# Kernel optimization log

Measured on AMD Instinct MI355X. Metric: run time of the kernel, lower is better.

Reference implementation:

```python
import jax, jax.numpy as jnp
import numpy as np


def _resize_axis(x, axis, out_size):
    # PyTorch bilinear interpolate, align_corners=False, no antialias (half-pixel centers)
    in_size = x.shape[axis]
    src = (jnp.arange(out_size) + 0.5) * (in_size / out_size) - 0.5
    src = jnp.clip(src, 0.0, in_size - 1.0)
    lo = jnp.floor(src).astype(jnp.int32)
    hi = jnp.minimum(lo + 1, in_size - 1)
    w = (src - lo).astype(x.dtype)
    shp = [1] * x.ndim
    shp[axis] = out_size
    w = w.reshape(shp)
    return jnp.take(x, lo, axis=axis) * (1 - w) + jnp.take(x, hi, axis=axis) * w


def _bilinear(x, h, w):
    return _resize_axis(_resize_axis(x, 2, h), 3, w)


def _unfold3(x):
    # F.unfold(kernel_size=3, padding=1) -> [B, C, 9, H*W], kernel offsets row-major
    B, C, H, W = x.shape
    xp = jnp.pad(x, ((0, 0), (0, 0), (1, 1), (1, 1)))
    pats = jnp.stack([xp[:, :, dy:dy + H, dx:dx + W] for dy in range(3) for dx in range(3)], axis=2)
    return pats.reshape(B, C, 9, H * W)


def setup_inputs() -> dict:
    key = jax.random.key(0)
    ks = jax.random.split(key, 7)
    B, C, H, W = 4, 64, 192, 192
    return {
        "x": jax.random.normal(ks[0], (B, C, H, W), jnp.float32),
        "gn_weight": jnp.ones((C,), jnp.float32) + 0.1 * jax.random.normal(ks[1], (C,), jnp.float32),
        "gn_bias": 0.1 * jax.random.normal(ks[2], (C,), jnp.float32),
        "w1": jax.random.normal(ks[3], (2 * C, C), jnp.float32) / np.sqrt(C).astype(np.float32),
        "b1": 0.01 * jax.random.normal(ks[4], (2 * C,), jnp.float32),
        "w2": jax.random.normal(ks[5], (C, 2 * C), jnp.float32) / np.sqrt(2 * C).astype(np.float32),
        "b2": 0.01 * jax.random.normal(ks[6], (C,), jnp.float32),
    }


def reference(x, gn_weight, gn_bias, w1, b1, w2, b2):
    B, C, H, W = x.shape
    MIN_CONN, MAX_CONN, THRESHOLD, POWER = 1, 16, 0.3, 2
    KSQ = 9
    K_MAX = min(MAX_CONN, KSQ)
    EPS_NORM = 1e-12

    x_down = _bilinear(x, H // 2, W // 2)
    x_du = _bilinear(x_down, H, W)
    df = jnp.abs(x - x_du).sum(1, keepdims=True)            # [B,1,H,W]
    dmin = df.reshape(B, -1).min(1).reshape(B, 1, 1, 1)
    dmax = df.reshape(B, -1).max(1).reshape(B, 1, 1, 1)
    dfp = ((df - dmin) / (dmax - dmin + 1e-8)) ** POWER
    mask = (dfp > THRESHOLD).astype(x.dtype)
    conn = MIN_CONN + jnp.clip(jnp.round(dfp * (MAX_CONN - MIN_CONN)), 0) * mask
    counts = conn.reshape(B, H * W)                          # [B,HW]
    process = counts > 1

    # ---- per-pixel cosine similarity to 3x3 neighborhood ----
    patches = _unfold3(x)                                    # [B,C,9,HW]
    x_flat = x.reshape(B, C, H * W)
    xn = x_flat / jnp.maximum(jnp.linalg.norm(x_flat, axis=1, keepdims=True), EPS_NORM)
    pn = patches / jnp.maximum(jnp.linalg.norm(patches, axis=1, keepdims=True), EPS_NORM)
    sim = jnp.einsum('bcn,bckn->bkn', xn, pn)                # [B,9,HW]

    # ---- adaptive top-k (k = min(count, 9)) + exp-softmax weighted sum of raw patches ----
    order = jnp.argsort(-sim, axis=1)                        # descending over the 9 neighbors
    sim_s = jnp.take_along_axis(sim, order, axis=1)
    pat_s = jnp.take_along_axis(patches, jnp.broadcast_to(order[:, None], patches.shape), axis=2)
    k = jnp.minimum(counts, K_MAX)                           # [B,HW]
    keep = (jnp.arange(KSQ)[None, :, None] < k[:, None, :]).astype(x.dtype)
    wts = jnp.exp(sim_s) * keep
    wts = wts / jnp.maximum(wts.sum(1, keepdims=True), EPS_NORM)
    weighted = jnp.einsum('bckn,bkn->bcn', pat_s, wts)       # [B,C,HW]
    output = jnp.where(process[:, None, :], weighted, x_flat).reshape(B, C, H, W)

    # ---- GroupNorm(32, C) on identity ----
    G = 32
    xg = x.reshape(B, G, C // G, H, W)
    mu = xg.mean((2, 3, 4), keepdims=True)
    var = xg.var((2, 3, 4), keepdims=True)
    nx = ((xg - mu) / jnp.sqrt(var + 1e-5)).reshape(B, C, H, W)
    norm_x = nx * gn_weight[None, :, None, None] + gn_bias[None, :, None, None]

    enhanced = output + norm_x
    # ---- conv_ffn: 1x1 conv C->2C, ReLU, 1x1 conv 2C->C ----
    h1 = jax.nn.relu(jnp.einsum('oc,bchw->bohw', w1, enhanced) + b1[None, :, None, None])
    ffn = jnp.einsum('oc,bchw->bohw', w2, h1) + b2[None, :, None, None]
    return enhanced + ffn
```

## Files before the change

### kernel.cpp

```cpp
#include <hip/hip_runtime.h>
#include <hip/hip_bf16.h>

#define BB 4
#define CC 64
#define HH 192
#define WW 192
#define HWSZ (HH*WW)
#define HD 96
#define WD 96
#define GG 32
#define FTH 512
#define FPX 128
#define FBPB (HWSZ/FPX)
#define PBLK 128
#define BPB (HWSZ/PBLK)

typedef short short8 __attribute__((ext_vector_type(8)));
typedef float f32x4  __attribute__((ext_vector_type(4)));

__device__ __forceinline__ unsigned short f2bf(float f) {
    unsigned u = __float_as_uint(f);
    return (unsigned short)((u + 0x7FFFu + ((u >> 16) & 1u)) >> 16);
}
__device__ __forceinline__ float bf2f(unsigned short s) {
    return __uint_as_float(((unsigned)s) << 16);
}
__device__ __forceinline__ unsigned pk2(float a, float b) {
    return (unsigned)f2bf(a) | ((unsigned)f2bf(b) << 16);
}
__device__ __forceinline__ short8 u4s8(uint4 u) {
    union { uint4 a; short8 b; } cvt; cvt.a = u; return cvt.b;
}

__device__ __forceinline__ int swz1152(int bid) {
    return (bid & 7) * 144 + (bid >> 3);
}

__global__ __launch_bounds__(512) void k_init(const float* __restrict__ w1,
                                              const float* __restrict__ w2,
                                              unsigned* __restrict__ wf,
                                              float* __restrict__ gnacc,
                                              unsigned* __restrict__ mm) {
    int tid = threadIdx.x;
    if (blockIdx.x == 0) {
        if (tid < 256) gnacc[tid] = 0.f;
        if (tid < 2*BB) mm[tid] = (tid & 1) ? 0u : 0x7F800000u;
    }
    int i = blockIdx.x*512 + tid;
    if (i < 4096) {
        float2 v = ((const float2*)w1)[i];
        int j = i >> 5, cp = i & 31, c0 = cp << 1;
        int fi = ((j >> 4) << 1) + (c0 >> 5);
        int ln = (((c0 & 31) >> 3) << 4) + (j & 15);
        wf[fi*256 + ln*4 + (cp & 3)] = pk2(v.x, v.y);
    } else {
        int i2 = i - 4096;
        float2 v = ((const float2*)w2)[i2];
        int c = i2 >> 6, jp = i2 & 63, j0 = jp << 1;
        int fi = ((j0 >> 5) << 2) + (c >> 4);
        int ln = (((j0 & 31) >> 3) << 4) + (c & 15);
        wf[4096 + fi*256 + ln*4 + (jp & 3)] = pk2(v.x, v.y);
    }
}

__global__ __launch_bounds__(256) void k_pre(const float* __restrict__ x,
                                             float* __restrict__ df,
                                             float* __restrict__ nrm,
                                             float* __restrict__ gnacc,
                                             unsigned* __restrict__ mm) {
    __shared__ float sgn[64];
    __shared__ float wmn[4], wmx[4];
    int tid = threadIdx.x;
    if (tid < 64) sgn[tid] = 0.f;
    __syncthreads();

    int virt = swz1152(blockIdx.x);
    int b = virt / BPB;
    int pb = (virt % BPB) * PBLK;
    int wave = tid >> 6, lane = tid & 63;
    int oct = lane >> 3, grp = lane & 7;
    int p0 = pb + wave*32 + grp*4;
    int h = p0 / WW, w0 = p0 % WW;

    float hs = fminf(fmaxf(0.5f*(float)h - 0.25f, 0.f), 95.f);
    int hl = (int)hs; int hh2 = min(hl+1, 95); float fh = hs - (float)hl;
    int r0 = 2*hl, r1 = 2*hh2;

    int t0 = min(max(w0/2 - 1, 0), 92);
    float wc[4][4];
    #pragma unroll
    for (int i = 0; i < 4; ++i) {
        float wsr = fminf(fmaxf(0.5f*(float)(w0+i) - 0.25f, 0.f), 95.f);
        int wl = (int)wsr; int wh = min(wl+1, 95); float fw = wsr - (float)wl;
        int kl = wl - t0, kh = wh - t0;
        #pragma unroll
        for (int k = 0; k < 4; ++k)
            wc[i][k] = ((k==kl) ? (1.f-fw) : 0.f) + ((k==kh) ? fw : 0.f);
    }

    const float* xb = x + (size_t)b*CC*HWSZ;
    float d[4]  = {0.f,0.f,0.f,0.f};
    float qn[4] = {0.f,0.f,0.f,0.f};
    float gs[4] = {0.f,0.f,0.f,0.f};
    float gq[4] = {0.f,0.f,0.f,0.f};
    #pragma unroll
    for (int cc = 0; cc < 8; ++cc) {
        const float* pc = xb + (size_t)(oct*8 + cc)*HWSZ;
        float4 xc = *(const float4*)(pc + h*WW + w0);
        const float* pa = pc + r0*WW + 2*t0;
        const float* pq = pc + r1*WW + 2*t0;
        float T[4];
        #pragma unroll
        for (int k = 0; k < 4; ++k) {
            float2 a0 = *(const float2*)(pa + 2*k);
            float2 a1 = *(const float2*)(pa + WW + 2*k);
            float2 c0 = *(const float2*)(pq + 2*k);
            float2 c1 = *(const float2*)(pq + WW + 2*k);
            float xdA = 0.25f*((a0.x + a1.x) + (a0.y + a1.y));
            float xdB = 0.25f*((c0.x + c1.x) + (c0.y + c1.y));
            T[k] = (1.f-fh)*xdA + fh*xdB;
        }
        float xv[4] = {xc.x, xc.y, xc.z, xc.w};
        float sch = 0.f, qch = 0.f;
        #pragma unroll
        for (int i = 0; i < 4; ++i) {
            float du = (wc[i][0]*T[0] + wc[i][1]*T[1]) + (wc[i][2]*T[2] + wc[i][3]*T[3]);
            d[i] += fabsf(xv[i] - du);
            float x2 = xv[i]*xv[i];
            qn[i] += x2;
            sch += xv[i];
            qch += x2;
        }
        gs[cc>>1] += sch;
        gq[cc>>1] += qch;
    }
    #pragma unroll
    for (int o = 8; o <= 32; o <<= 1) {
        #pragma unroll
        for (int i = 0; i < 4; ++i) {
            d[i]  += __shfl_xor(d[i], o);
            qn[i] += __shfl_xor(qn[i], o);
        }
    }
    if (oct == 0) {
        *(float4*)(df  + (size_t)b*HWSZ + p0) = make_float4(d[0], d[1], d[2], d[3]);
        *(float4*)(nrm + (size_t)b*HWSZ + p0) =
            make_float4(sqrtf(qn[0]), sqrtf(qn[1]), sqrtf(qn[2]), sqrtf(qn[3]));
    }
    float mn = fminf(fminf(d[0], d[1]), fminf(d[2], d[3]));
    float mx = fmaxf(fmaxf(d[0], d[1]), fmaxf(d[2], d[3]));
    #pragma unroll
    for (int o = 1; o < 64; o <<= 1) {
        mn = fminf(mn, __shfl_xor(mn, o));
        mx = fmaxf(mx, __shfl_xor(mx, o));
    }
    if (lane == 0) { wmn[wave] = mn; wmx[wave] = mx; }
    #pragma unroll
    for (int o = 1; o <= 4; o <<= 1) {
        #pragma unroll
        for (int j = 0; j < 4; ++j) {
            gs[j] += __shfl_xor(gs[j], o);
            gq[j] += __shfl_xor(gq[j], o);
        }
    }
    if (grp == 0) {
        #pragma unroll
        for (int j = 0; j < 4; ++j) {
            atomicAdd(&sgn[2*(oct*4+j)],   gs[j]);
            atomicAdd(&sgn[2*(oct*4+j)+1], gq[j]);
        }
    }
    __syncthreads();
    if (tid < 64) atomicAdd(&gnacc[(size_t)b*64 + tid], sgn[tid]);
    if (tid == 0) {
        float bmn = fminf(fminf(wmn[0], wmn[1]), fminf(wmn[2], wmn[3]));
        float bmx = fmaxf(fmaxf(wmx[0], wmx[1]), fmaxf(wmx[2], wmx[3]));
        atomicMin(&mm[2*b],   __float_as_uint(bmn));
        atomicMax(&mm[2*b+1], __float_as_uint(bmx));
    }
}

__global__ __launch_bounds__(FTH, 4) void k_fused(const float* __restrict__ x,
                                                  const float* __restrict__ df,
                                                  const float* __restrict__ nrm,
                                                  const unsigned* __restrict__ mm,
                                                  const float* __restrict__ gnacc,
                                                  const float* __restrict__ gw,
                                                  const float* __restrict__ gb,
                                                  const unsigned* __restrict__ wf,
                                                  const float* __restrict__ b1,
                                                  const float* __restrict__ b2,
                                                  float* __restrict__ out) {
    __shared__ __align__(16) unsigned char lds[24576];
    unsigned* se = (unsigned*)lds;
    unsigned* sh = (unsigned*)(lds + 16384);
    float* gnv = (float*)(lds + 16384);

    int tid = threadIdx.x;
    int wv = tid >> 6, lane = tid & 63;
    int q = lane >> 4, m = lane & 15;

    int virt = swz1152(blockIdx.x);
    int b = virt / FBPB;
    int pb = (virt % FBPB) * FPX;
    int pxl = wv*16 + m;
    int p = pb + pxl;
    int h = p / WW, w = p % WW;
    int cbase = q*16;

    if (tid < 32) {
        float n = 2.f*HWSZ;
        float mu  = gnacc[(size_t)b*64 + 2*tid] / n;
        float var = gnacc[(size_t)b*64 + 2*tid + 1] / n - mu*mu;
        gnv[2*tid]   = mu;
        gnv[2*tid+1] = rsqrtf(var + 1e-5f);
    }
    __syncthreads();

    float dmin = __uint_as_float(mm[2*b]);
    float dmax = __uint_as_float(mm[2*b+1]);
    float dfp = (df[b*HWSZ+p] - dmin) / (dmax - dmin + 1e-8f);
    dfp = dfp * dfp;
    bool maskv = dfp > 0.3f;
    float conn = 1.f + (maskv ? fmaxf(rintf(dfp * 15.f), 0.f) : 0.f);
    bool process = conn > 1.f;
    int kk = (int)fminf(conn, 9.f);

    const float* xb = x + (size_t)b*CC*HWSZ + p;
    const int dhv[9] = {-1,-1,-1, 0,0,0, 1,1,1};
    const int dwv[9] = {-1, 0, 1,-1,0,1,-1,0,1};
    bool valid[9]; int offc[9];
    #pragma unroll
    for (int j = 0; j < 9; ++j) {
        int hn = h + dhv[j], wn = w + dwv[j];
        valid[j] = (hn >= 0) && (hn < HH) && (wn >= 0) && (wn < WW);
        offc[j] = valid[j] ? (dhv[j]*WW + dwv[j]) : 0;
    }
    float wtc[9];
    #pragma unroll
    for (int j = 0; j < 9; ++j) wtc[j] = 0.f;

    if (process) {
        float dot[9];
        #pragma unroll
        for (int j = 0; j < 9; ++j) dot[j] = 0.f;
        #pragma unroll 2
        for (int cc = 0; cc < 16; ++cc) {
            const float* pc = xb + (size_t)(cbase + cc)*HWSZ;
            float xc = pc[0];
            #pragma unroll
            for (int j = 0; j < 9; ++j)
                dot[j] += xc * pc[offc[j]];
        }
        #pragma unroll
        for (int j = 0; j < 9; ++j) {
            dot[j] += __shfl_xor(dot[j], 16);
            dot[j] += __shfl_xor(dot[j], 32);
        }
        float nc = fmaxf(nrm[b*HWSZ+p], 1e-12f);
        float sim[9];
        #pragma unroll
        for (int j = 0; j < 9; ++j) {
            float nj = fmaxf(nrm[b*HWSZ+p+offc[j]], 1e-12f);
            sim[j] = valid[j] ? dot[j] / (nc * nj) : 0.f;
        }
        float S = 0.f;
        float wt[9];
        #pragma unroll
        for (int j = 0; j < 9; ++j) {
            int rank = 0;
            #pragma unroll
            for (int l = 0; l < 9; ++l)
                rank += (sim[l] > sim[j]) || (sim[l] == sim[j] && l < j);
            float ex = (rank < kk) ? expf(sim[j]) : 0.f;
            wt[j] = ex; S += ex;
        }
        float inv = 1.f / fmaxf(S, 1e-12f);
        #pragma unroll
        for (int j = 0; j < 9; ++j)
            wtc[j] = valid[j] ? wt[j] * inv : 0.f;
    }

    float e[16];
    for (int cc = 0; cc < 16; ++cc) {
        int c = cbase + cc;
        const float* pc = xb + (size_t)c*HWSZ;
        float xc = pc[0];
        float oc;
        if (process) {
            float a = 0.f;
            #pragma unroll
            for (int j = 0; j < 9; ++j)
                a += wtc[j] * pc[offc[j]];
            oc = a;
        } else oc = xc;
        int g = c >> 1;
        float mu = gnv[2*g], is = gnv[2*g+1];
        e[cc] = oc + (xc - mu) * is * gw[c] + gb[c];
    }

    {
        int kc = q >> 1, qo = q & 1;
        unsigned* dst = se + (wv*2 + kc)*256;
        int la = 32*qo + m;
        uint4 ua, ub;
        ua.x = pk2(e[0],e[1]);  ua.y = pk2(e[2],e[3]);
        ua.z = pk2(e[4],e[5]);  ua.w = pk2(e[6],e[7]);
        ub.x = pk2(e[8],e[9]);  ub.y = pk2(e[10],e[11]);
        ub.z = pk2(e[12],e[13]); ub.w = pk2(e[14],e[15]);
        *(uint4*)(dst + la*4)      = ua;
        *(uint4*)(dst + (la+16)*4) = ub;
    }
    __syncthreads();

    const unsigned* wf1g = wf;
    const unsigned* wf2g = wf + 4096;
    int n16 = m;
    float b1v[8], b2v[4];
    #pragma unroll
    for (int nt = 0; nt < 8; ++nt) b1v[nt] = b1[nt*16 + n16];
    #pragma unroll
    for (int n2 = 0; n2 < 4; ++n2) b2v[n2] = b2[n2*16 + n16];

    uint4 a0 = *(uint4*)(se + (wv*2+0)*256 + lane*4);
    uint4 a1 = *(uint4*)(se + (wv*2+1)*256 + lane*4);
    f32x4 D1[8];
    #pragma unroll
    for (int nt = 0; nt < 8; ++nt) D1[nt] = (f32x4){0.f,0.f,0.f,0.f};
    #pragma unroll
    for (int nt = 0; nt < 8; ++nt) {
        uint4 bk0 = *(const uint4*)(wf1g + (nt*2+0)*256 + lane*4);
        uint4 bk1 = *(const uint4*)(wf1g + (nt*2+1)*256 + lane*4);
        D1[nt] = __builtin_amdgcn_mfma_f32_16x16x32_bf16(u4s8(a0), u4s8(bk0), D1[nt], 0, 0, 0);
        D1[nt] = __builtin_amdgcn_mfma_f32_16x16x32_bf16(u4s8(a1), u4s8(bk1), D1[nt], 0, 0, 0);
    }
    f32x4 D2[4];
    #pragma unroll
    for (int n2 = 0; n2 < 4; ++n2) D2[n2] = (f32x4){0.f,0.f,0.f,0.f};
    unsigned* shwv = sh + wv*256;
    unsigned short* shw = (unsigned short*)shwv;
    for (int kc2 = 0; kc2 < 4; ++kc2) {
        #pragma unroll
        for (int h2 = 0; h2 < 2; ++h2) {
            int nt = kc2*2 + h2;
            #pragma unroll
            for (int r = 0; r < 4; ++r) {
                float hval = fmaxf(D1[nt][r] + b1v[nt], 0.f);
                int mrow = q*4 + r;
                int k = h2*16 + n16;
                shw[((k >> 3)*16 + mrow)*8 + (k & 7)] = f2bf(hval);
            }
        }
        uint4 ah = *(uint4*)(shwv + lane*4);
        #pragma unroll
        for (int n2 = 0; n2 < 4; ++n2) {
            uint4 bb = *(const uint4*)(wf2g + (kc2*4 + n2)*256 + lane*4);
            D2[n2] = __builtin_amdgcn_mfma_f32_16x16x32_bf16(u4s8(ah), u4s8(bb), D2[n2], 0, 0, 0);
        }
    }
    float vals[4][4];
    unsigned short* seu = (unsigned short*)se;
    #pragma unroll
    for (int n2 = 0; n2 < 4; ++n2) {
        int c = n2*16 + n16;
        int kc = c >> 5, qq = (c & 31) >> 3, jj = c & 7;
        #pragma unroll
        for (int r = 0; r < 4; ++r) {
            int pxt = q*4 + r;
            float resid = bf2f(seu[((wv*2+kc)*64 + qq*16 + pxt)*8 + jj]);
            vals[n2][r] = D2[n2][r] + resid + b2v[n2];
        }
    }
    __syncthreads();

    float* stg = (float*)lds;
    float* outb = out + (size_t)b*CC*HWSZ;
    #pragma unroll
    for (int g = 0; g < 2; ++g) {
        #pragma unroll
        for (int hn2 = 0; hn2 < 2; ++hn2) {
            int n2 = 2*g + hn2;
            int row = (n2 & 1)*16 + n16;
            float4 v4 = make_float4(vals[n2][0], vals[n2][1], vals[n2][2], vals[n2][3]);
            *(float4*)&stg[row*132 + wv*16 + q*4] = v4;
        }
        __syncthreads();
        #pragma unroll
        for (int rr = 0; rr < 2; ++rr) {
            int r0 = (wv*2 + rr)*2 + (lane >> 5);
            int px4 = (lane & 31) * 4;
            float4 v = *(float4*)&stg[r0*132 + px4];
            *(float4*)&outb[(size_t)(g*32 + r0)*HWSZ + pb + px4] = v;
        }
        if (g == 0) __syncthreads();
    }
}

extern "C" void kernel_launch(void* const* d_in, const int* in_sizes, int n_in,
                              void* d_out, int out_size, void* d_ws, size_t ws_size,
                              hipStream_t stream) {
    const float* x  = (const float*)d_in[0];
    const float* gw = (const float*)d_in[1];
    const float* gb = (const float*)d_in[2];
    const float* w1 = (const float*)d_in[3];
    const float* b1 = (const float*)d_in[4];
    const float* w2 = (const float*)d_in[5];
    const float* b2 = (const float*)d_in[6];
    float* out = (float*)d_out;

    float* df    = (float*)d_ws;
    float* nrm   = df + 147456;
    float* gnacc = nrm + 147456;
    unsigned* mm = (unsigned*)(gnacc + 256);
    unsigned* wf = mm + 8;

    k_init <<<16, 512, 0, stream>>>(w1, w2, wf, gnacc, mm);
    k_pre  <<<BB*BPB, 256, 0, stream>>>(x, df, nrm, gnacc, mm);
    k_fused<<<BB*FBPB, FTH, 0, stream>>>(x, df, nrm, mm, gnacc, gw, gb,
                                         wf, b1, b2, out);
}
```

Baseline: 188.7 us.

## Replace three-kernel pipeline with a cooperative row-per-block megakernel and grid sync

Merges weight packing, detail/statistics pass and the fused FFN pass into one cooperative kernel with a grid-wide barrier. Each block handles one image row, stages input rows into shared memory through a triple buffer, and precomputes the nine neighbour dot products. These are kept in registers across the barrier so the second phase does not reload them. A two-kernel fallback using global scratch runs if the cooperative launch fails. The aim is to cut launch overhead and redundant global reads. The risks are grid-sync cost, lower occupancy from 47KB of shared memory, and the requirement that all 768 blocks be co-resident.

Measured after the change: 340.2 us. 1.8x slower.

```diff
diff --git a/kernel.cpp b/kernel.cpp
--- a/kernel.cpp
+++ b/kernel.cpp
@@ -1,19 +1,13 @@
 #include <hip/hip_runtime.h>
-#include <hip/hip_bf16.h>
+#include <hip/hip_cooperative_groups.h>
+
+namespace cg = cooperative_groups;
 
 #define BB 4
 #define CC 64
 #define HH 192
 #define WW 192
 #define HWSZ (HH*WW)
-#define HD 96
-#define WD 96
-#define GG 32
-#define FTH 512
-#define FPX 128
-#define FBPB (HWSZ/FPX)
-#define PBLK 128
-#define BPB (HWSZ/PBLK)
 
 typedef short short8 __attribute__((ext_vector_type(8)));
 typedef float f32x4  __attribute__((ext_vector_type(4)));
@@ -32,181 +26,193 @@
     union { uint4 a; short8 b; } cvt; cvt.a = u; return cvt.b;
 }
 
-__device__ __forceinline__ int swz1152(int bid) {
-    return (bid & 7) * 144 + (bid >> 3);
-}
-
-__global__ __launch_bounds__(512) void k_init(const float* __restrict__ w1,
-                                              const float* __restrict__ w2,
-                                              unsigned* __restrict__ wf,
-                                              float* __restrict__ gnacc,
-                                              unsigned* __restrict__ mm) {
-    int tid = threadIdx.x;
-    if (blockIdx.x == 0) {
-        if (tid < 256) gnacc[tid] = 0.f;
-        if (tid < 2*BB) mm[tid] = (tid & 1) ? 0u : 0x7F800000u;
-    }
-    int i = blockIdx.x*512 + tid;
-    if (i < 4096) {
-        float2 v = ((const float2*)w1)[i];
-        int j = i >> 5, cp = i & 31, c0 = cp << 1;
-        int fi = ((j >> 4) << 1) + (c0 >> 5);
-        int ln = (((c0 & 31) >> 3) << 4) + (j & 15);
-        wf[fi*256 + ln*4 + (cp & 3)] = pk2(v.x, v.y);
-    } else {
-        int i2 = i - 4096;
-        float2 v = ((const float2*)w2)[i2];
-        int c = i2 >> 6, jp = i2 & 63, j0 = jp << 1;
-        int fi = ((j0 >> 5) << 2) + (c >> 4);
-        int ln = (((j0 & 31) >> 3) << 4) + (c & 15);
-        wf[4096 + fi*256 + ln*4 + (jp & 3)] = pk2(v.x, v.y);
-    }
-}
-
-__global__ __launch_bounds__(256) void k_pre(const float* __restrict__ x,
-                                             float* __restrict__ df,
-                                             float* __restrict__ nrm,
-                                             float* __restrict__ gnacc,
-                                             unsigned* __restrict__ mm) {
-    __shared__ float sgn[64];
-    __shared__ float wmn[4], wmx[4];
-    int tid = threadIdx.x;
+#define SM_BYTES 47392
+
+template<int COOP>
+__device__ __forceinline__ void phaseA(const float* __restrict__ x,
+                                       const float* __restrict__ w1,
+                                       const float* __restrict__ w2,
+                                       unsigned* __restrict__ wf,
+                                       float* __restrict__ nrmg,
+                                       float* __restrict__ gnacc,
+                                       unsigned* __restrict__ mmmin,
+                                       unsigned* __restrict__ mmmax,
+                                       float* __restrict__ dfg,
+                                       float* __restrict__ dotsg,
+                                       unsigned char* smem,
+                                       int b, int h, float* dd, float& dfv) {
+    float (*rbA)[8][192] = (float (*)[8][192])smem;
+    float* sgn = (float*)(smem + 47104);
+    float* red = (float*)(smem + 47360);
+    int tid = threadIdx.x, lane = tid & 63, wv = tid >> 6;
     if (tid < 64) sgn[tid] = 0.f;
-    __syncthreads();
-
-    int virt = swz1152(blockIdx.x);
-    int b = virt / BPB;
-    int pb = (virt % BPB) * PBLK;
-    int wave = tid >> 6, lane = tid & 63;
-    int oct = lane >> 3, grp = lane & 7;
-    int p0 = pb + wave*32 + grp*4;
-    int h = p0 / WW, w0 = p0 % WW;
+
+    if (blockIdx.x < 16) {
+        #pragma unroll
+        for (int rep = 0; rep < 2; ++rep) {
+            int i = blockIdx.x*512 + rep*256 + tid;
+            if (i < 4096) {
+                float2 v = ((const float2*)w1)[i];
+                int j = i >> 5, cp = i & 31, c0 = cp << 1;
+                int fi = ((j >> 4) << 1) + (c0 >> 5);
+                int ln = (((c0 & 31) >> 3) << 4) + (j & 15);
+                wf[fi*256 + ln*4 + (cp & 3)] = pk2(v.x, v.y);
+            } else {
+                int i2 = i - 4096;
+                float2 v = ((const float2*)w2)[i2];
+                int c = i2 >> 6, jp = i2 & 63, j0 = jp << 1;
+                int fi = ((j0 >> 5) << 2) + (c >> 4);
+                int ln = (((j0 & 31) >> 3) << 4) + (c & 15);
+                wf[4096 + fi*256 + ln*4 + (jp & 3)] = pk2(v.x, v.y);
+            }
+        }
+    }
 
     float hs = fminf(fmaxf(0.5f*(float)h - 0.25f, 0.f), 95.f);
     int hl = (int)hs; int hh2 = min(hl+1, 95); float fh = hs - (float)hl;
-    int r0 = 2*hl, r1 = 2*hh2;
-
-    int t0 = min(max(w0/2 - 1, 0), 92);
-    float wc[4][4];
+    int R[4] = {2*hl, 2*hl+1, 2*hh2, 2*hh2+1};
+    int su = 0, cs = 0, sd = 0;
     #pragma unroll
-    for (int i = 0; i < 4; ++i) {
-        float wsr = fminf(fmaxf(0.5f*(float)(w0+i) - 0.25f, 0.f), 95.f);
-        int wl = (int)wsr; int wh = min(wl+1, 95); float fw = wsr - (float)wl;
-        int kl = wl - t0, kh = wh - t0;
-        #pragma unroll
-        for (int k = 0; k < 4; ++k)
-            wc[i][k] = ((k==kl) ? (1.f-fw) : 0.f) + ((k==kh) ? fw : 0.f);
-    }
-
+    for (int s = 3; s >= 0; --s) {
+        if (R[s] == h-1) su = s;
+        if (R[s] == h)   cs = s;
+        if (R[s] == h+1) sd = s;
+    }
     const float* xb = x + (size_t)b*CC*HWSZ;
-    float d[4]  = {0.f,0.f,0.f,0.f};
-    float qn[4] = {0.f,0.f,0.f,0.f};
-    float gs[4] = {0.f,0.f,0.f,0.f};
-    float gq[4] = {0.f,0.f,0.f,0.f};
+
+    int w = tid;
+    int cl = max(w-1, 0), cr = min(w+1, WW-1);
+    float wsr = fminf(fmaxf(0.5f*(float)w - 0.25f, 0.f), 95.f);
+    int wl = (int)wsr; int wh = min(wl+1, 95); float fw = wsr - (float)wl;
+    int c2l = 2*wl, c2h = 2*wh;
     #pragma unroll
-    for (int cc = 0; cc < 8; ++cc) {
-        const float* pc = xb + (size_t)(oct*8 + cc)*HWSZ;
-        float4 xc = *(const float4*)(pc + h*WW + w0);
-        const float* pa = pc + r0*WW + 2*t0;
-        const float* pq = pc + r1*WW + 2*t0;
-        float T[4];
-        #pragma unroll
-        for (int k = 0; k < 4; ++k) {
-            float2 a0 = *(const float2*)(pa + 2*k);
-            float2 a1 = *(const float2*)(pa + WW + 2*k);
-            float2 c0 = *(const float2*)(pq + 2*k);
-            float2 c1 = *(const float2*)(pq + WW + 2*k);
-            float xdA = 0.25f*((a0.x + a1.x) + (a0.y + a1.y));
-            float xdB = 0.25f*((c0.x + c1.x) + (c0.y + c1.y));
-            T[k] = (1.f-fh)*xdA + fh*xdB;
-        }
-        float xv[4] = {xc.x, xc.y, xc.z, xc.w};
-        float sch = 0.f, qch = 0.f;
-        #pragma unroll
-        for (int i = 0; i < 4; ++i) {
-            float du = (wc[i][0]*T[0] + wc[i][1]*T[1]) + (wc[i][2]*T[2] + wc[i][3]*T[3]);
-            d[i] += fabsf(xv[i] - du);
-            float x2 = xv[i]*xv[i];
-            qn[i] += x2;
-            sch += xv[i];
-            qch += x2;
-        }
-        gs[cc>>1] += sch;
-        gq[cc>>1] += qch;
-    }
+    for (int j = 0; j < 9; ++j) dd[j] = 0.f;
+    dfv = 0.f;
+
+    int st = tid - 192;
+    int srow = st >> 3, scid = st & 7;
+    bool stg = tid >= 192;
+    float4 pf[6];
+
+    if (stg) {
+        const float* b0 = xb + (size_t)(0 + (srow>>2))*HWSZ + R[srow&3]*WW;
+        #pragma unroll
+        for (int k = 0; k < 6; ++k) pf[k] = *(const float4*)(b0 + (scid+8*k)*4);
+        #pragma unroll
+        for (int k = 0; k < 6; ++k) *(float4*)&rbA[0][srow][(scid+8*k)*4] = pf[k];
+        const float* b1p = xb + (size_t)(2 + (srow>>2))*HWSZ + R[srow&3]*WW;
+        #pragma unroll
+        for (int k = 0; k < 6; ++k) pf[k] = *(const float4*)(b1p + (scid+8*k)*4);
+    }
+    __syncthreads();
+
+    for (int it = 0; it < 32; ++it) {
+        int cur = it % 3, nxt = (it+1) % 3;
+        int c = 2*it;
+        if (stg) {
+            #pragma unroll
+            for (int k = 0; k < 6; ++k) *(float4*)&rbA[nxt][srow][(scid+8*k)*4] = pf[k];
+            if (it + 2 < 32) {
+                const float* bp = xb + (size_t)(2*(it+2) + (srow>>2))*HWSZ + R[srow&3]*WW;
+                #pragma unroll
+                for (int k = 0; k < 6; ++k) pf[k] = *(const float4*)(bp + (scid+8*k)*4);
+            }
+        }
+        float s_ = 0.f, q_ = 0.f;
+        if (tid < 192) {
+            #pragma unroll
+            for (int sub = 0; sub < 2; ++sub) {
+                const float* r0 = rbA[cur][4*sub+0];
+                const float* r1 = rbA[cur][4*sub+1];
+                const float* r2 = rbA[cur][4*sub+2];
+                const float* r3 = rbA[cur][4*sub+3];
+                float2 a0 = *(const float2*)&r0[c2l];
+                float2 a1 = *(const float2*)&r1[c2l];
+                float2 a2 = *(const float2*)&r2[c2l];
+                float2 a3 = *(const float2*)&r3[c2l];
+                float Tl = (1.f-fh)*(0.25f*((a0.x+a1.x)+(a0.y+a1.y)))
+                         +      fh *(0.25f*((a2.x+a3.x)+(a2.y+a3.y)));
+                a0 = *(const float2*)&r0[c2h];
+                a1 = *(const float2*)&r1[c2h];
+                a2 = *(const float2*)&r2[c2h];
+                a3 = *(const float2*)&r3[c2h];
+                float Th = (1.f-fh)*(0.25f*((a0.x+a1.x)+(a0.y+a1.y)))
+                         +      fh *(0.25f*((a2.x+a3.x)+(a2.y+a3.y)));
+                float du = (1.f-fw)*Tl + fw*Th;
+                const float* ru = rbA[cur][4*sub+su];
+                const float* rc = rbA[cur][4*sub+cs];
+                const float* rd = rbA[cur][4*sub+sd];
+                float xc = rc[w];
+                dfv += fabsf(xc - du);
+                dd[0] += xc*ru[cl]; dd[1] += xc*ru[w]; dd[2] += xc*ru[cr];
+                dd[3] += xc*rc[cl]; dd[4] += xc*xc;   dd[5] += xc*rc[cr];
+                dd[6] += xc*rd[cl]; dd[7] += xc*rd[w]; dd[8] += xc*rd[cr];
+                s_ += xc; q_ += xc*xc;
+            }
+        }
+        #pragma unroll
+        for (int o = 1; o <= 32; o <<= 1) {
+            s_ += __shfl_xor(s_, o);
+            q_ += __shfl_xor(q_, o);
+        }
+        if (lane == 0 && wv < 3) {
+            atomicAdd(&sgn[c],   s_);
+            atomicAdd(&sgn[c+1], q_);
+        }
+        __syncthreads();
+    }
+
+    if (tid < 192) {
+        nrmg[(size_t)b*HWSZ + h*WW + w] = sqrtf(dd[4]);
+        if (!COOP) {
+            dfg[(size_t)b*HWSZ + h*WW + w] = dfv;
+            #pragma unroll
+            for (int j = 0; j < 9; ++j)
+                dotsg[((size_t)(b*9 + j))*HWSZ + h*WW + w] = dd[j];
+        }
+    }
+    float mn = (tid < 192) ? dfv : 3.4e38f;
+    float mx = (tid < 192) ? dfv : 0.f;
     #pragma unroll
-    for (int o = 8; o <= 32; o <<= 1) {
-        #pragma unroll
-        for (int i = 0; i < 4; ++i) {
-            d[i]  += __shfl_xor(d[i], o);
-            qn[i] += __shfl_xor(qn[i], o);
-        }
-    }
-    if (oct == 0) {
-        *(float4*)(df  + (size_t)b*HWSZ + p0) = make_float4(d[0], d[1], d[2], d[3]);
-        *(float4*)(nrm + (size_t)b*HWSZ + p0) =
-            make_float4(sqrtf(qn[0]), sqrtf(qn[1]), sqrtf(qn[2]), sqrtf(qn[3]));
-    }
-    float mn = fminf(fminf(d[0], d[1]), fminf(d[2], d[3]));
-    float mx = fmaxf(fmaxf(d[0], d[1]), fmaxf(d[2], d[3]));
-    #pragma unroll
-    for (int o = 1; o < 64; o <<= 1) {
+    for (int o = 1; o <= 32; o <<= 1) {
         mn = fminf(mn, __shfl_xor(mn, o));
         mx = fmaxf(mx, __shfl_xor(mx, o));
     }
-    if (lane == 0) { wmn[wave] = mn; wmx[wave] = mx; }
-    #pragma unroll
-    for (int o = 1; o <= 4; o <<= 1) {
-        #pragma unroll
-        for (int j = 0; j < 4; ++j) {
-            gs[j] += __shfl_xor(gs[j], o);
-            gq[j] += __shfl_xor(gq[j], o);
-        }
-    }
-    if (grp == 0) {
-        #pragma unroll
-        for (int j = 0; j < 4; ++j) {
-            atomicAdd(&sgn[2*(oct*4+j)],   gs[j]);
-            atomicAdd(&sgn[2*(oct*4+j)+1], gq[j]);
-        }
-    }
+    if (lane == 0) { red[wv] = mn; red[4+wv] = mx; }
     __syncthreads();
     if (tid < 64) atomicAdd(&gnacc[(size_t)b*64 + tid], sgn[tid]);
     if (tid == 0) {
-        float bmn = fminf(fminf(wmn[0], wmn[1]), fminf(wmn[2], wmn[3]));
-        float bmx = fmaxf(fmaxf(wmx[0], wmx[1]), fmaxf(wmx[2], wmx[3]));
-        atomicMin(&mm[2*b],   __float_as_uint(bmn));
-        atomicMax(&mm[2*b+1], __float_as_uint(bmx));
-    }
-}
-
-__global__ __launch_bounds__(FTH, 4) void k_fused(const float* __restrict__ x,
-                                                  const float* __restrict__ df,
-                                                  const float* __restrict__ nrm,
-                                                  const unsigned* __restrict__ mm,
-                                                  const float* __restrict__ gnacc,
-                                                  const float* __restrict__ gw,
-                                                  const float* __restrict__ gb,
-                                                  const unsigned* __restrict__ wf,
-                                                  const float* __restrict__ b1,
-                                                  const float* __restrict__ b2,
-                                                  float* __restrict__ out) {
-    __shared__ __align__(16) unsigned char lds[24576];
-    unsigned* se = (unsigned*)lds;
-    unsigned* sh = (unsigned*)(lds + 16384);
-    float* gnv = (float*)(lds + 16384);
-
-    int tid = threadIdx.x;
-    int wv = tid >> 6, lane = tid & 63;
+        float bmn = fminf(fminf(red[0], red[1]), red[2]);
+        float bmx = fmaxf(fmaxf(red[4], red[5]), red[6]);
+        atomicMin(&mmmin[b], __float_as_uint(bmn));
+        atomicMax(&mmmax[b], __float_as_uint(bmx));
+    }
+}
+
+template<int COOP>
+__device__ __forceinline__ void phaseB(const float* __restrict__ x,
+                                       const float* __restrict__ gw,
+                                       const float* __restrict__ gb,
+                                       const unsigned* __restrict__ wf,
+                                       const float* __restrict__ b1,
+                                       const float* __restrict__ b2,
+                                       const float* __restrict__ nrmg,
+                                       const float* __restrict__ gnacc,
+                                       const unsigned* __restrict__ mmmin,
+                                       const unsigned* __restrict__ mmmax,
+                                       const float* __restrict__ dfg,
+                                       const float* __restrict__ dotsg,
+                                       float* __restrict__ out,
+                                       unsigned char* smem,
+                                       int b, int h, float* dd, float dfv) {
+    float (*rb2)[6][192] = (float (*)[6][192])smem;
+    float (*nrm3)[192]   = (float (*)[192])(smem + 13824);
+    unsigned* eu          = (unsigned*)(smem + 18432);
+    unsigned short* es    = (unsigned short*)(smem + 18432);
+    unsigned* sh          = (unsigned*)(smem + 43008);
+    float* gnv            = (float*)(smem + 47104);
+    int tid = threadIdx.x, lane = tid & 63, wv = tid >> 6;
     int q = lane >> 4, m = lane & 15;
-
-    int virt = swz1152(blockIdx.x);
-    int b = virt / FBPB;
-    int pb = (virt % FBPB) * FPX;
-    int pxl = wv*16 + m;
-    int p = pb + pxl;
-    int h = p / WW, w = p % WW;
-    int cbase = q*16;
 
     if (tid < 32) {
         float n = 2.f*HWSZ;
@@ -215,185 +221,250 @@
         gnv[2*tid]   = mu;
         gnv[2*tid+1] = rsqrtf(var + 1e-5f);
     }
+    if (tid < 144) {
+        int r = tid/48, c4 = (tid%48)*4;
+        int hsrc = min(max(h-1+r, 0), HH-1);
+        *(float4*)&nrm3[r][c4] = *(const float4*)&nrmg[(size_t)b*HWSZ + hsrc*WW + c4];
+    }
+
+    int st = tid - 192;
+    bool stg = tid >= 192;
+    float4 pf[5];
+    auto stage_load = [&](int pair) {
+        #pragma unroll
+        for (int k = 0; k < 5; ++k) {
+            int idx = st + 64*k;
+            if (idx < 288) {
+                int row6 = idx/48, c4 = (idx%48)*4;
+                int chO = row6/3, rr = row6 - 3*chO;
+                int hsrc = min(max(h-1+rr, 0), HH-1);
+                pf[k] = *(const float4*)(x + ((size_t)b*CC + 2*pair + chO)*HWSZ + hsrc*WW + c4);
+            }
+        }
+    };
+    auto stage_write = [&](int buf) {
+        #pragma unroll
+        for (int k = 0; k < 5; ++k) {
+            int idx = st + 64*k;
+            if (idx < 288) {
+                int row6 = idx/48, c4 = (idx%48)*4;
+                *(float4*)&rb2[buf][row6][c4] = pf[k];
+            }
+        }
+    };
+    if (stg) { stage_load(0); stage_write(0); stage_load(1); }
     __syncthreads();
 
-    float dmin = __uint_as_float(mm[2*b]);
-    float dmax = __uint_as_float(mm[2*b+1]);
-    float dfp = (df[b*HWSZ+p] - dmin) / (dmax - dmin + 1e-8f);
-    dfp = dfp * dfp;
-    bool maskv = dfp > 0.3f;
-    float conn = 1.f + (maskv ? fmaxf(rintf(dfp * 15.f), 0.f) : 0.f);
-    bool process = conn > 1.f;
-    int kk = (int)fminf(conn, 9.f);
-
-    const float* xb = x + (size_t)b*CC*HWSZ + p;
-    const int dhv[9] = {-1,-1,-1, 0,0,0, 1,1,1};
-    const int dwv[9] = {-1, 0, 1,-1,0,1,-1,0,1};
-    bool valid[9]; int offc[9];
-    #pragma unroll
-    for (int j = 0; j < 9; ++j) {
-        int hn = h + dhv[j], wn = w + dwv[j];
-        valid[j] = (hn >= 0) && (hn < HH) && (wn >= 0) && (wn < WW);
-        offc[j] = valid[j] ? (dhv[j]*WW + dwv[j]) : 0;
-    }
+    int w = tid;
+    int cl = max(w-1, 0), cr = min(w+1, WW-1);
     float wtc[9];
     #pragma unroll
     for (int j = 0; j < 9; ++j) wtc[j] = 0.f;
-
-    if (process) {
-        float dot[9];
-        #pragma unroll
-        for (int j = 0; j < 9; ++j) dot[j] = 0.f;
-        #pragma unroll 2
-        for (int cc = 0; cc < 16; ++cc) {
-            const float* pc = xb + (size_t)(cbase + cc)*HWSZ;
-            float xc = pc[0];
+    bool process = false;
+    if (tid < 192) {
+        if (!COOP) {
+            dfv = dfg[(size_t)b*HWSZ + h*WW + w];
             #pragma unroll
             for (int j = 0; j < 9; ++j)
-                dot[j] += xc * pc[offc[j]];
-        }
-        #pragma unroll
-        for (int j = 0; j < 9; ++j) {
-            dot[j] += __shfl_xor(dot[j], 16);
-            dot[j] += __shfl_xor(dot[j], 32);
-        }
-        float nc = fmaxf(nrm[b*HWSZ+p], 1e-12f);
-        float sim[9];
-        #pragma unroll
-        for (int j = 0; j < 9; ++j) {
-            float nj = fmaxf(nrm[b*HWSZ+p+offc[j]], 1e-12f);
-            sim[j] = valid[j] ? dot[j] / (nc * nj) : 0.f;
-        }
-        float S = 0.f;
-        float wt[9];
-        #pragma unroll
-        for (int j = 0; j < 9; ++j) {
-            int rank = 0;
-            #pragma unroll
-            for (int l = 0; l < 9; ++l)
-                rank += (sim[l] > sim[j]) || (sim[l] == sim[j] && l < j);
-            float ex = (rank < kk) ? expf(sim[j]) : 0.f;
-            wt[j] = ex; S += ex;
-        }
-        float inv = 1.f / fmaxf(S, 1e-12f);
-        #pragma unroll
-        for (int j = 0; j < 9; ++j)
-            wtc[j] = valid[j] ? wt[j] * inv : 0.f;
-    }
-
-    float e[16];
-    for (int cc = 0; cc < 16; ++cc) {
-        int c = cbase + cc;
-        const float* pc = xb + (size_t)c*HWSZ;
-        float xc = pc[0];
-        float oc;
+                dd[j] = dotsg[((size_t)(b*9 + j))*HWSZ + h*WW + w];
+        }
+        float dmin = __uint_as_float(mmmin[b]);
+        float dmax = __uint_as_float(mmmax[b]);
+        float dfp = (dfv - dmin) / (dmax - dmin + 1e-8f);
+        dfp = dfp * dfp;
+        float conn = 1.f + ((dfp > 0.3f) ? fmaxf(rintf(dfp * 15.f), 0.f) : 0.f);
+        process = conn > 1.f;
+        int kk = (int)fminf(conn, 9.f);
+        const int dhv[9] = {-1,-1,-1, 0,0,0, 1,1,1};
+        const int dwv[9] = {-1, 0, 1,-1,0,1,-1,0,1};
         if (process) {
-            float a = 0.f;
+            bool valid[9];
+            #pragma unroll
+            for (int j = 0; j < 9; ++j) {
+                int hn = h + dhv[j], wn = w + dwv[j];
+                valid[j] = (hn >= 0) && (hn < HH) && (wn >= 0) && (wn < WW);
+            }
+            float nc = fmaxf(nrm3[1][w], 1e-12f);
+            float sim[9];
+            #pragma unroll
+            for (int j = 0; j < 9; ++j) {
+                int wn = min(max(w + dwv[j], 0), WW-1);
+                float nj = fmaxf(nrm3[1+dhv[j]][wn], 1e-12f);
+                sim[j] = valid[j] ? dd[j] / (nc * nj) : 0.f;
+            }
+            float S = 0.f, wt[9];
+            #pragma unroll
+            for (int j = 0; j < 9; ++j) {
+                int rank = 0;
+                #pragma unroll
+                for (int l = 0; l < 9; ++l)
+                    rank += (sim[l] > sim[j]) || (sim[l] == sim[j] && l < j);
+                float ex = (rank < kk) ? expf(sim[j]) : 0.f;
+                wt[j] = ex; S += ex;
+            }
+            float inv = 1.f / fmaxf(S, 1e-12f);
             #pragma unroll
             for (int j = 0; j < 9; ++j)
-                a += wtc[j] * pc[offc[j]];
-            oc = a;
-        } else oc = xc;
-        int g = c >> 1;
-        float mu = gnv[2*g], is = gnv[2*g+1];
-        e[cc] = oc + (xc - mu) * is * gw[c] + gb[c];
-    }
-
-    {
-        int kc = q >> 1, qo = q & 1;
-        unsigned* dst = se + (wv*2 + kc)*256;
-        int la = 32*qo + m;
-        uint4 ua, ub;
-        ua.x = pk2(e[0],e[1]);  ua.y = pk2(e[2],e[3]);
-        ua.z = pk2(e[4],e[5]);  ua.w = pk2(e[6],e[7]);
-        ub.x = pk2(e[8],e[9]);  ub.y = pk2(e[10],e[11]);
-        ub.z = pk2(e[12],e[13]); ub.w = pk2(e[14],e[15]);
-        *(uint4*)(dst + la*4)      = ua;
-        *(uint4*)(dst + (la+16)*4) = ub;
-    }
-    __syncthreads();
+                wtc[j] = valid[j] ? wt[j] * inv : 0.f;
+        }
+    }
+
+    int tile = w >> 4, mrow = w & 15;
+    for (int it = 0; it < 32; ++it) {
+        int cur = it % 3, nxt = (it+1) % 3;
+        int c = 2*it;
+        if (stg) {
+            stage_write(nxt);
+            if (it + 2 < 32) stage_load(it+2);
+        }
+        if (tid < 192) {
+            float ev[2];
+            float mu = gnv[2*it], is = gnv[2*it+1];
+            #pragma unroll
+            for (int sub = 0; sub < 2; ++sub) {
+                const float* ru = rb2[cur][3*sub+0];
+                const float* rc = rb2[cur][3*sub+1];
+                const float* rd = rb2[cur][3*sub+2];
+                float xc = rc[w];
+                float oc;
+                if (process) {
+                    oc = wtc[0]*ru[cl] + wtc[1]*ru[w] + wtc[2]*ru[cr]
+                       + wtc[3]*rc[cl] + wtc[4]*xc    + wtc[5]*rc[cr]
+                       + wtc[6]*rd[cl] + wtc[7]*rd[w] + wtc[8]*rd[cr];
+                } else oc = xc;
+                int cc = c + sub;
+                ev[sub] = oc + (xc - mu) * is * gw[cc] + gb[cc];
+            }
+            int la = 32*((c>>4)&1) + 16*((c>>3)&1) + mrow;
+            eu[tile*512 + (c>>5)*256 + la*4 + ((c>>1)&3)] = pk2(ev[0], ev[1]);
+        }
+        __syncthreads();
+    }
 
     const unsigned* wf1g = wf;
     const unsigned* wf2g = wf + 4096;
-    int n16 = m;
     float b1v[8], b2v[4];
     #pragma unroll
-    for (int nt = 0; nt < 8; ++nt) b1v[nt] = b1[nt*16 + n16];
+    for (int nt = 0; nt < 8; ++nt) b1v[nt] = b1[nt*16 + m];
     #pragma unroll
-    for (int n2 = 0; n2 < 4; ++n2) b2v[n2] = b2[n2*16 + n16];
-
-    uint4 a0 = *(uint4*)(se + (wv*2+0)*256 + lane*4);
-    uint4 a1 = *(uint4*)(se + (wv*2+1)*256 + lane*4);
-    f32x4 D1[8];
-    #pragma unroll
-    for (int nt = 0; nt < 8; ++nt) D1[nt] = (f32x4){0.f,0.f,0.f,0.f};
-    #pragma unroll
-    for (int nt = 0; nt < 8; ++nt) {
-        uint4 bk0 = *(const uint4*)(wf1g + (nt*2+0)*256 + lane*4);
-        uint4 bk1 = *(const uint4*)(wf1g + (nt*2+1)*256 + lane*4);
-        D1[nt] = __builtin_amdgcn_mfma_f32_16x16x32_bf16(u4s8(a0), u4s8(bk0), D1[nt], 0, 0, 0);
-        D1[nt] = __builtin_amdgcn_mfma_f32_16x16x32_bf16(u4s8(a1), u4s8(bk1), D1[nt], 0, 0, 0);
-    }
-    f32x4 D2[4];
-    #pragma unroll
-    for (int n2 = 0; n2 < 4; ++n2) D2[n2] = (f32x4){0.f,0.f,0.f,0.f};
+    for (int n2 = 0; n2 < 4; ++n2) b2v[n2] = b2[n2*16 + m];
     unsigned* shwv = sh + wv*256;
     unsigned short* shw = (unsigned short*)shwv;
-    for (int kc2 = 0; kc2 < 4; ++kc2) {
-        #pragma unroll
-        for (int h2 = 0; h2 < 2; ++h2) {
-            int nt = kc2*2 + h2;
+    float* outb = out + (size_t)b*CC*HWSZ + h*WW;
+
+    for (int t3 = 0; t3 < 3; ++t3) {
+        int tl = wv*3 + t3;
+        uint4 a0 = *(uint4*)(eu + tl*512 + lane*4);
+        uint4 a1 = *(uint4*)(eu + tl*512 + 256 + lane*4);
+        f32x4 D1[8];
+        #pragma unroll
+        for (int nt = 0; nt < 8; ++nt) D1[nt] = (f32x4){0.f,0.f,0.f,0.f};
+        #pragma unroll
+        for (int nt = 0; nt < 8; ++nt) {
+            uint4 bk0 = *(const uint4*)(wf1g + (nt*2+0)*256 + lane*4);
+            uint4 bk1 = *(const uint4*)(wf1g + (nt*2+1)*256 + lane*4);
+            D1[nt] = __builtin_amdgcn_mfma_f32_16x16x32_bf16(u4s8(a0), u4s8(bk0), D1[nt], 0, 0, 0);
+            D1[nt] = __builtin_amdgcn_mfma_f32_16x16x32_bf16(u4s8(a1), u4s8(bk1), D1[nt], 0, 0, 0);
+        }
+        f32x4 D2[4];
+        #pragma unroll
+        for (int n2 = 0; n2 < 4; ++n2) D2[n2] = (f32x4){0.f,0.f,0.f,0.f};
+        for (int kc2 = 0; kc2 < 4; ++kc2) {
+            #pragma unroll
+            for (int h2 = 0; h2 < 2; ++h2) {
+                int nt = kc2*2 + h2;
+                #pragma unroll
+                for (int r = 0; r < 4; ++r) {
+                    float hval = fmaxf(D1[nt][r] + b1v[nt], 0.f);
+                    int k = h2*16 + m;
+                    shw[((k >> 3)*16 + (q*4+r))*8 + (k & 7)] = f2bf(hval);
+                }
+            }
+            uint4 ah = *(uint4*)(shwv + lane*4);
+            #pragma unroll
+            for (int n2 = 0; n2 < 4; ++n2) {
+                uint4 bb = *(const uint4*)(wf2g + (kc2*4 + n2)*256 + lane*4);
+                D2[n2] = __builtin_amdgcn_mfma_f32_16x16x32_bf16(u4s8(ah), u4s8(bb), D2[n2], 0, 0, 0);
+            }
+        }
+        #pragma unroll
+        for (int n2 = 0; n2 < 4; ++n2) {
+            int c = n2*16 + m;
+            int kc = c >> 5, qq = (c & 31) >> 3, jj = c & 7;
+            float4 vout;
+            float* vp = (float*)&vout;
             #pragma unroll
             for (int r = 0; r < 4; ++r) {
-                float hval = fmaxf(D1[nt][r] + b1v[nt], 0.f);
-                int mrow = q*4 + r;
-                int k = h2*16 + n16;
-                shw[((k >> 3)*16 + mrow)*8 + (k & 7)] = f2bf(hval);
-            }
-        }
-        uint4 ah = *(uint4*)(shwv + lane*4);
-        #pragma unroll
-        for (int n2 = 0; n2 < 4; ++n2) {
-            uint4 bb = *(const uint4*)(wf2g + (kc2*4 + n2)*256 + lane*4);
-            D2[n2] = __builtin_amdgcn_mfma_f32_16x16x32_bf16(u4s8(ah), u4s8(bb), D2[n2], 0, 0, 0);
-        }
-    }
-    float vals[4][4];
-    unsigned short* seu = (unsigned short*)se;
-    #pragma unroll
-    for (int n2 = 0; n2 < 4; ++n2) {
-        int c = n2*16 + n16;
-        int kc = c >> 5, qq = (c & 31) >> 3, jj = c & 7;
-        #pragma unroll
-        for (int r = 0; r < 4; ++r) {
-            int pxt = q*4 + r;
-            float resid = bf2f(seu[((wv*2+kc)*64 + qq*16 + pxt)*8 + jj]);
-            vals[n2][r] = D2[n2][r] + resid + b2v[n2];
-        }
-    }
-    __syncthreads();
-
-    float* stg = (float*)lds;
-    float* outb = out + (size_t)b*CC*HWSZ;
-    #pragma unroll
-    for (int g = 0; g < 2; ++g) {
-        #pragma unroll
-        for (int hn2 = 0; hn2 < 2; ++hn2) {
-            int n2 = 2*g + hn2;
-            int row = (n2 & 1)*16 + n16;
-            float4 v4 = make_float4(vals[n2][0], vals[n2][1], vals[n2][2], vals[n2][3]);
-            *(float4*)&stg[row*132 + wv*16 + q*4] = v4;
-        }
-        __syncthreads();
-        #pragma unroll
-        for (int rr = 0; rr < 2; ++rr) {
-            int r0 = (wv*2 + rr)*2 + (lane >> 5);
-            int px4 = (lane & 31) * 4;
-            float4 v = *(float4*)&stg[r0*132 + px4];
-            *(float4*)&outb[(size_t)(g*32 + r0)*HWSZ + pb + px4] = v;
-        }
-        if (g == 0) __syncthreads();
-    }
+                float resid = bf2f(es[((tl*2+kc)*64 + qq*16 + q*4 + r)*8 + jj]);
+                vp[r] = D2[n2][r] + resid + b2v[n2];
+            }
+            *(float4*)&outb[(size_t)c*HWSZ + tl*16 + q*4] = vout;
+        }
+    }
+}
+
+__global__ __launch_bounds__(256, 3) void k_megaC(const float* __restrict__ x,
+                                                  const float* __restrict__ gw,
+                                                  const float* __restrict__ gb,
+                                                  const float* __restrict__ w1,
+                                                  const float* __restrict__ w2,
+                                                  const float* __restrict__ b1,
+                                                  const float* __restrict__ b2,
+                                                  float* __restrict__ nrmg,
+                                                  float* __restrict__ gnacc,
+                                                  unsigned* __restrict__ mmmin,
+                                                  unsigned* __restrict__ mmmax,
+                                                  unsigned* __restrict__ wf,
+                                                  float* __restrict__ out) {
+    __shared__ __align__(16) unsigned char smem[SM_BYTES];
+    int virt = (blockIdx.x & 7) * 96 + (blockIdx.x >> 3);
+    int b = virt / HH, h = virt % HH;
+    float dd[9]; float dfv;
+    phaseA<1>(x, w1, w2, wf, nrmg, gnacc, mmmin, mmmax,
+              nullptr, nullptr, smem, b, h, dd, dfv);
+    __threadfence();
+    cg::this_grid().sync();
+    phaseB<1>(x, gw, gb, wf, b1, b2, nrmg, gnacc, mmmin, mmmax,
+              nullptr, nullptr, out, smem, b, h, dd, dfv);
+}
+
+__global__ __launch_bounds__(256) void k_pA(const float* __restrict__ x,
+                                            const float* __restrict__ w1,
+                                            const float* __restrict__ w2,
+                                            unsigned* __restrict__ wf,
+                                            float* __restrict__ nrmg,
+                                            float* __restrict__ gnacc,
+                                            unsigned* __restrict__ mmmin,
+                                            unsigned* __restrict__ mmmax,
+                                            float* __restrict__ dfg,
+                                            float* __restrict__ dotsg) {
+    __shared__ __align__(16) unsigned char smem[SM_BYTES];
+    int virt = (blockIdx.x & 7) * 96 + (blockIdx.x >> 3);
+    int b = virt / HH, h = virt % HH;
+    float dd[9]; float dfv;
+    phaseA<0>(x, w1, w2, wf, nrmg, gnacc, mmmin, mmmax, dfg, dotsg,
+              smem, b, h, dd, dfv);
+}
+
+__global__ __launch_bounds__(256) void k_pB(const float* __restrict__ x,
+                                            const float* __restrict__ gw,
+                                            const float* __restrict__ gb,
+                                            const unsigned* __restrict__ wf,
+                                            const float* __restrict__ b1,
+                                            const float* __restrict__ b2,
+                                            const float* __restrict__ nrmg,
+                                            const float* __restrict__ gnacc,
+                                            const unsigned* __restrict__ mmmin,
+                                            const unsigned* __restrict__ mmmax,
+                                            const float* __restrict__ dfg,
+                                            const float* __restrict__ dotsg,
+                                            float* __restrict__ out) {
+    __shared__ __align__(16) unsigned char smem[SM_BYTES];
+    int virt = (blockIdx.x & 7) * 96 + (blockIdx.x >> 3);
+    int b = virt / HH, h = virt % HH;
+    float dd[9]; float dfv = 0.f;
+    phaseB<0>(x, gw, gb, wf, b1, b2, nrmg, gnacc, mmmin, mmmax,
+              dfg, dotsg, out, smem, b, h, dd, dfv);
 }
 
 extern "C" void kernel_launch(void* const* d_in, const int* in_sizes, int n_in,
@@ -408,14 +479,30 @@
     const float* b2 = (const float*)d_in[6];
     float* out = (float*)d_out;
 
-    float* df    = (float*)d_ws;
-    float* nrm   = df + 147456;
-    float* gnacc = nrm + 147456;
-    unsigned* mm = (unsigned*)(gnacc + 256);
-    unsigned* wf = mm + 8;
-
-    k_init <<<16, 512, 0, stream>>>(w1, w2, wf, gnacc, mm);
-    k_pre  <<<BB*BPB, 256, 0, stream>>>(x, df, nrm, gnacc, mm);
-    k_fused<<<BB*FBPB, FTH, 0, stream>>>(x, df, nrm, mm, gnacc, gw, gb,
-                                         wf, b1, b2, out);
-}
+    float* nrm      = (float*)d_ws;
+    float* gnacc    = nrm + 147456;
+    unsigned* mmmax = (unsigned*)(gnacc + 256);
+    unsigned* mmmin = mmmax + 4;
+    unsigned* wf    = mmmin + 4;
+    float* df       = (float*)(wf + 8192);
+    float* dots     = df + 147456;
+    const size_t NEED = (size_t)(147456 + 256 + 8 + 8192 + 147456 + 9*147456) * 4;
+    bool big = ws_size >= NEED;
+
+    hipMemsetAsync(gnacc, 0, (256 + 4) * sizeof(float), stream);
+    hipMemsetAsync(mmmin, 0xFF, 4 * sizeof(unsigned), stream);
+
+    void* kargs[] = {(void*)&x, (void*)&gw, (void*)&gb, (void*)&w1, (void*)&w2,
+                     (void*)&b1, (void*)&b2, (void*)&nrm, (void*)&gnacc,
+                     (void*)&mmmin, (void*)&mmmax, (void*)&wf, (void*)&out};
+    hipError_t err = hipLaunchCooperativeKernel((const void*)k_megaC,
+                                                dim3(BB*HH), dim3(256),
+                                                kargs, 0, stream);
+    if (err != hipSuccess && big) {
+        (void)hipGetLastError();
+        k_pA<<<BB*HH, 256, 0, stream>>>(x, w1, w2, wf, nrm, gnacc, mmmin, mmmax,
+                                        df, dots);
+        k_pB<<<BB*HH, 256, 0, stream>>>(x, gw, gb, wf, b1, b2, nrm, gnacc,
+                                        mmmin, mmmax, df, dots, out);
+    }
+}
```
